# Kernel optimization log

Measured on AMD Instinct MI355X. Metric: run time of the kernel, lower is better.

Reference implementation:

```python
import jax, jax.numpy as jnp
import numpy as np

D_MODEL = 1024
D_STATE = 128
EXPAND = 2
HEADDIM = 64
D_CONV = 4
VAR_NUM = 3
D_INNER = EXPAND * D_MODEL            # 2048
NHEADS = D_INNER // HEADDIM           # 32
CONV_DIM = D_INNER + 2 * D_STATE      # 2304 (x, B, C share the conv)
D_IN_PROJ = 2 * D_INNER + 2 * D_STATE + NHEADS  # 4384


def setup_inputs() -> dict:
    key = jax.random.key(0)
    ks = jax.random.split(key, 10)
    s = 0.02
    B, L = 4, 2048
    return {
        "h_prev": jax.random.normal(ks[0], (B, L, D_MODEL), jnp.float32),
        "emb_next": jax.random.normal(ks[1], (B, L, D_MODEL), jnp.float32),
        "norm_w": jnp.ones((D_MODEL,), jnp.float32),
        "proj_W": jax.random.normal(ks[2], (D_MODEL, 2 * D_MODEL), jnp.float32) * s,
        "proj_b": jnp.zeros((D_MODEL,), jnp.float32),
        "in_proj_W": jax.random.normal(ks[3], (D_IN_PROJ, D_MODEL), jnp.float32) * s,
        "conv_w": jax.random.normal(ks[4], (CONV_DIM, D_CONV), jnp.float32) * s,
        "conv_b": jnp.zeros((CONV_DIM,), jnp.float32),
        "dt_bias": jax.random.uniform(ks[5], (NHEADS,), jnp.float32) * 0.1,
        "A_log": jnp.log(jnp.arange(1, NHEADS + 1, dtype=jnp.float32)),
        "D": jnp.ones((NHEADS,), jnp.float32),
        "gnorm_w": jnp.ones((D_INNER,), jnp.float32),
        "out_proj_W": jax.random.normal(ks[6], (D_MODEL, D_INNER), jnp.float32) * s,
        "dec_W": jax.random.normal(ks[7], (VAR_NUM, D_MODEL), jnp.float32) * s,
        "dec_b": jnp.zeros((VAR_NUM,), jnp.float32),
    }


def rmsnorm(x, w, eps=1e-6):
    xf = x.astype(jnp.float32)
    v = jnp.mean(jnp.square(xf), axis=-1, keepdims=True)
    return w * (xf * jax.lax.rsqrt(v + eps)).astype(x.dtype)


def gated_rmsnorm(y, z, w, eps=1e-5):
    y = y * jax.nn.silu(z)
    v = jnp.mean(jnp.square(y.astype(jnp.float32)), axis=-1, keepdims=True)
    return w * (y.astype(jnp.float32) * jax.lax.rsqrt(v + eps)).astype(y.dtype)


def mamba2(u, in_proj_W, conv_w, conv_b, dt_bias, A_log, D, gnorm_w, out_proj_W):
    B, L, _ = u.shape
    zxbcdt = u @ in_proj_W.T  # [B,L,D_IN_PROJ]
    z, xBC, dt = jnp.split(zxbcdt, [D_INNER, D_INNER + CONV_DIM], axis=-1)
    # causal depthwise conv over time
    lhs = jnp.moveaxis(xBC, -1, 1)               # [B,C,L]
    rhs = conv_w[:, None, :]                     # [C,1,K]
    conv = jax.lax.conv_general_dilated(lhs, rhs, (1,), [(D_CONV - 1, 0)],
                                        feature_group_count=CONV_DIM)
    xBC = jax.nn.silu(jnp.moveaxis(conv, 1, -1) + conv_b)
    x, Bm, Cm = jnp.split(xBC, [D_INNER, D_INNER + D_STATE], axis=-1)
    x = x.reshape(B, L, NHEADS, HEADDIM)         # [B,L,H,P]
    dt = jax.nn.softplus(dt + dt_bias)           # [B,L,H]
    A = -jnp.exp(A_log)                          # [H]
    dA = jnp.exp(dt * A)                         # [B,L,H]

    def step(state, inp):
        dA_t, dt_t, B_t, C_t, x_t = inp          # [B,H],[B,H],[B,N],[B,N],[B,H,P]
        state = state * dA_t[..., None, None] + (dt_t[..., None, None] * x_t[..., None]) * B_t[:, None, None, :]
        y_t = jnp.einsum('bhpn,bn->bhp', state, C_t)
        return state, y_t

    init = jnp.zeros((B, NHEADS, HEADDIM, D_STATE), u.dtype)
    xs = (jnp.moveaxis(dA, 1, 0), jnp.moveaxis(dt, 1, 0), jnp.moveaxis(Bm, 1, 0),
          jnp.moveaxis(Cm, 1, 0), jnp.moveaxis(x, 1, 0))
    _, y = jax.lax.scan(step, init, xs)          # y: [L,B,H,P]
    y = jnp.moveaxis(y, 0, 1) + D[None, None, :, None] * x
    y = y.reshape(B, L, D_INNER)
    y = gated_rmsnorm(y, z, gnorm_w)
    return y @ out_proj_W.T                      # [B,L,D_MODEL]


def reference(h_prev, emb_next, norm_w, proj_W, proj_b, in_proj_W, conv_w, conv_b,
              dt_bias, A_log, D, gnorm_w, out_proj_W, dec_W, dec_b):
    combined = jnp.concatenate([rmsnorm(h_prev, norm_w), rmsnorm(emb_next, norm_w)], axis=-1)
    h_prime = combined @ proj_W.T + proj_b       # [B,L,D_MODEL]
    h_k = mamba2(h_prime, in_proj_W, conv_w, conv_b, dt_bias, A_log, D, gnorm_w, out_proj_W)
    output = h_k @ dec_W.T + dec_b               # [B,L,VAR_NUM]
    return output, h_k
```

## Files before the change

kernel.cpp:

```cpp
#include <hip/hip_runtime.h>
#include <stdint.h>

#define T_TOK 8192
#define SEQL  2048
#define DM    1024
#define DI    2048
#define DSTATE 128
#define NH    32
#define HD    64
#define CONVD 2304
#define DINP  4384
#define LD_ZX 4480
#define QC    64
#define NCH   32

typedef __attribute__((ext_vector_type(8))) __bf16 bfrag;
typedef __attribute__((ext_vector_type(8))) short s16x8;
typedef __attribute__((ext_vector_type(4))) float f32x4;

__device__ __forceinline__ float bf2f(unsigned short u){
  return __uint_as_float(((unsigned)u) << 16);
}
__device__ __forceinline__ unsigned short f2bf(float f){
  unsigned u = __float_as_uint(f);
  unsigned r = (u + 0x7FFFu + ((u >> 16) & 1u)) >> 16;
  return (unsigned short)r;
}

__device__ __forceinline__ void gl_lds16(const unsigned short* g, unsigned short* l){
  __builtin_amdgcn_global_load_lds(
      (const __attribute__((address_space(1))) void*)g,
      (__attribute__((address_space(3))) void*)l,
      16, 0, 0);
}
__device__ __forceinline__ void gl_lds4(const float* g, float* l){
  __builtin_amdgcn_global_load_lds(
      (const __attribute__((address_space(1))) void*)g,
      (__attribute__((address_space(3))) void*)l,
      4, 0, 0);
}

__global__ __launch_bounds__(256) void prep_kernel(const float* __restrict__ s0,
                                                   const float* __restrict__ s1,
                                                   const float* __restrict__ s2,
                                                   unsigned short* __restrict__ d0,
                                                   unsigned short* __restrict__ d1,
                                                   unsigned short* __restrict__ d2,
                                                   const float* __restrict__ a,
                                                   const float* __restrict__ b,
                                                   const float* __restrict__ w,
                                                   unsigned short* __restrict__ out){
  int blk = blockIdx.x;
  int tid = threadIdx.x;
  if (blk < 8576){
    const float* src; unsigned short* dst; int i, srcn4;
    if (blk < 2048){
      src = s0; dst = d0; i = blk * 256 + tid; srcn4 = DM * DI / 4;
    } else if (blk < 6528){
      src = s1; dst = d1; i = (blk - 2048) * 256 + tid; srcn4 = DINP * DM / 4;
    } else {
      src = s2; dst = d2; i = (blk - 6528) * 256 + tid; srcn4 = DM * DI / 4;
    }
    ushort4 o;
    if (i < srcn4){
      float4 v = ((const float4*)src)[i];
      o.x = f2bf(v.x); o.y = f2bf(v.y); o.z = f2bf(v.z); o.w = f2bf(v.w);
    } else {
      o.x = o.y = o.z = o.w = 0;
    }
    *(ushort4*)(dst + (size_t)i * 4) = o;
    return;
  }
  int t = blk - 8576;
  float4 va = *(const float4*)(a + (size_t)t * DM + tid * 4);
  float4 vb = *(const float4*)(b + (size_t)t * DM + tid * 4);
  float sa = va.x*va.x + va.y*va.y + va.z*va.z + va.w*va.w;
  float sb = vb.x*vb.x + vb.y*vb.y + vb.z*vb.z + vb.w*vb.w;
  #pragma unroll
  for (int o = 32; o; o >>= 1){ sa += __shfl_down(sa, o); sb += __shfl_down(sb, o); }
  __shared__ float reda[4], redb[4];
  int wv = tid >> 6, lane = tid & 63;
  if (!lane){ reda[wv] = sa; redb[wv] = sb; }
  __syncthreads();
  float ta = reda[0] + reda[1] + reda[2] + reda[3];
  float tb = redb[0] + redb[1] + redb[2] + redb[3];
  float ra = rsqrtf(ta * (1.f/1024.f) + 1e-6f);
  float rb = rsqrtf(tb * (1.f/1024.f) + 1e-6f);
  float4 vw = *(const float4*)(w + tid * 4);
  unsigned short* o0 = out + (size_t)t * DI + tid * 4;
  o0[0] = f2bf(va.x*ra*vw.x); o0[1] = f2bf(va.y*ra*vw.y);
  o0[2] = f2bf(va.z*ra*vw.z); o0[3] = f2bf(va.w*ra*vw.w);
  unsigned short* o1 = o0 + DM;
  o1[0] = f2bf(vb.x*rb*vw.x); o1[1] = f2bf(vb.y*rb*vw.y);
  o1[2] = f2bf(vb.z*rb*vw.z); o1[3] = f2bf(vb.w*rb*vw.w);
}

template<bool F32OUT>
__global__ __launch_bounds__(256) void gemm_bf16_kernel(const unsigned short* __restrict__ A,
                                                        const unsigned short* __restrict__ W,
                                                        void* __restrict__ Cv,
                                                        const float* __restrict__ bias,
                                                        int M, int N, int K, int ldc){
  __shared__ unsigned short As[128 * 64];
  __shared__ unsigned short Bs[128 * 64];
  const int nN = N >> 7;
  int bid = blockIdx.x;
  const int cpx = gridDim.x >> 3;
  bid = (bid & 7) * cpx + (bid >> 3);
  const int tm = bid / nN, tn = bid % nN;
  const int tid = threadIdx.x;
  const int wv = tid >> 6, lane = tid & 63;
  const int wm = wv >> 1, wn = wv & 1;
  const int rA = lane >> 3;
  const int cS = ((lane & 7) ^ rA) << 3;
  const size_t arow0 = (size_t)(tm * 128) * K;
  const size_t brow0 = (size_t)(tn * 128) * K;

  int aoff[4][2], boff[4][2];
  #pragma unroll
  for (int f = 0; f < 4; ++f)
    #pragma unroll
    for (int kk = 0; kk < 2; ++kk){
      int ar = wm*64 + f*16 + (lane & 15);
      int br = wn*64 + f*16 + (lane & 15);
      int u  = kk*4 + (lane >> 4);
      aoff[f][kk] = ar * 64 + ((u ^ (ar & 7)) << 3);
      boff[f][kk] = br * 64 + ((u ^ (br & 7)) << 3);
    }

  f32x4 zero4 = {0.f, 0.f, 0.f, 0.f};
  f32x4 acc[4][4];
  #pragma unroll
  for (int i = 0; i < 4; ++i)
    #pragma unroll
    for (int j = 0; j < 4; ++j) acc[i][j] = zero4;

  const int nK = K >> 6;
  for (int kt = 0; kt < nK; ++kt){
    const int k0 = kt << 6;
    if (kt) __syncthreads();
    #pragma unroll
    for (int i = 0; i < 4; ++i){
      int base = (wv * 4 + i) * 8;
      gl_lds16(A + arow0 + (size_t)(base + rA) * K + k0 + cS, &As[base * 64]);
      gl_lds16(W + brow0 + (size_t)(base + rA) * K + k0 + cS, &Bs[base * 64]);
    }
    __syncthreads();
    #pragma unroll
    for (int kk = 0; kk < 2; ++kk){
      bfrag af[4], bfv[4];
      #pragma unroll
      for (int f = 0; f < 4; ++f){
        af[f]  = *reinterpret_cast<const bfrag*>(&As[aoff[f][kk]]);
        bfv[f] = *reinterpret_cast<const bfrag*>(&Bs[boff[f][kk]]);
      }
      #pragma unroll
      for (int fm = 0; fm < 4; ++fm)
        #pragma unroll
        for (int fn = 0; fn < 4; ++fn)
          acc[fm][fn] = __builtin_amdgcn_mfma_f32_16x16x32_bf16(af[fm], bfv[fn], acc[fm][fn], 0, 0, 0);
    }
  }
  const int r0 = (lane >> 4) * 4, ci = lane & 15;
  #pragma unroll
  for (int fm = 0; fm < 4; ++fm){
    #pragma unroll
    for (int fn = 0; fn < 4; ++fn){
      int col = tn*128 + wn*64 + fn*16 + ci;
      float bv = bias ? bias[col] : 0.f;
      #pragma unroll
      for (int r = 0; r < 4; ++r){
        int row = tm*128 + wm*64 + fm*16 + r0 + r;
        float val = acc[fm][fn][r] + bv;
        if (F32OUT) ((float*)Cv)[(size_t)row * ldc + col] = val;
        else        ((unsigned short*)Cv)[(size_t)row * ldc + col] = f2bf(val);
      }
    }
  }
}

__global__ __launch_bounds__(256) void convcum_kernel(const unsigned short* __restrict__ zx,
                                                      const float* __restrict__ cw,
                                                      const float* __restrict__ cb,
                                                      unsigned short* __restrict__ xbc,
                                                      const float* __restrict__ dtbias,
                                                      const float* __restrict__ alog,
                                                      float* __restrict__ cumT,
                                                      float* __restrict__ dtT,
                                                      float* __restrict__ decayG){
  int blk = blockIdx.x;
  int tid = threadIdx.x;
  if (blk < 4608){
    int c = (blk % 9) * 256 + tid;
    int tg = (blk / 9) * 16;
    int l0 = tg & (SEQL - 1);
    const unsigned short* base = zx + (size_t)tg * LD_ZX + DI + c;
    float v[19];
    #pragma unroll
    for (int i = 0; i < 19; ++i){
      int ll = l0 - 3 + i;
      v[i] = (ll >= 0) ? bf2f(base[(ptrdiff_t)(i - 3) * LD_ZX]) : 0.f;
    }
    float w0 = cw[c*4+0], w1 = cw[c*4+1], w2 = cw[c*4+2], w3 = cw[c*4+3];
    float cbv = cb[c];
    unsigned short* ob = xbc + (size_t)tg * CONVD + c;
    #pragma unroll
    for (int s = 0; s < 16; ++s){
      float acc = cbv + w0*v[s] + w1*v[s+1] + w2*v[s+2] + w3*v[s+3];
      float sv = acc / (1.f + expf(-acc));
      ob[(size_t)s * CONVD] = f2bf(sv);
    }
    return;
  }
  int gw = (blk - 4608) * 4 + (tid >> 6);
  int l = tid & 63;
  int c = gw & 31, h = (gw >> 5) & 31, b = gw >> 10;
  size_t t = (size_t)b * SEQL + c * QC + l;
  float xr = bf2f(zx[t * LD_ZX + 4352 + h]) + dtbias[h];
  float dt = (xr > 20.f) ? xr : log1pf(expf(xr));
  float A = -expf(alog[h]);
  float x = dt * A;
  #pragma unroll
  for (int d = 1; d < 64; d <<= 1){
    float y = __shfl_up(x, d);
    if (l >= d) x += y;
  }
  size_t o = ((size_t)(b * NH + h)) * SEQL + c * QC + l;
  cumT[o] = x;
  dtT[o] = dt;
  float tot = __shfl(x, 63);
  if (l == 0) decayG[(b * NH + h) * NCH + c] = expf(tot);
}

__global__ __launch_bounds__(256) void chunk_dS_kernel(const unsigned short* __restrict__ xbc,
                                                       const float* __restrict__ cumT,
                                                       const float* __restrict__ dtT,
                                                       unsigned short* __restrict__ dS){
  __shared__ unsigned short Xw[64 * 64];
  __shared__ unsigned short Bt[128 * 64];
  __shared__ float cumS[64], dtS[64];
  const int blk = blockIdx.x;
  const int c = blk & 31, h = (blk >> 5) & 31, b = blk >> 10;
  const int tid = threadIdx.x;
  const int wv = tid >> 6, l = tid & 63;
  const size_t tokB = (size_t)b * SEQL + c * QC;
  const int bh = b * NH + h;

  if (wv == 0) gl_lds4(cumT + (size_t)bh * SEQL + c * QC + l, cumS);
  if (wv == 1) gl_lds4(dtT  + (size_t)bh * SEQL + c * QC + l, dtS);

  const int j = tid >> 2, g4 = tid & 3;
  const unsigned short* xsrc = xbc + (tokB + j) * CONVD + h * HD + g4 * 16;
  s16x8 x0 = *(const s16x8*)xsrc, x1 = *(const s16x8*)(xsrc + 8);
  const unsigned short* bsrc = xbc + (tokB + j) * CONVD + DI + g4 * 32;
  s16x8 b0 = *(const s16x8*)bsrc,        b1 = *(const s16x8*)(bsrc + 8);
  s16x8 b2 = *(const s16x8*)(bsrc + 16), b3 = *(const s16x8*)(bsrc + 24);
  __syncthreads();

  float wj = expf(cumS[63] - cumS[j]) * dtS[j];
  const int jh = (j >> 3), jl = (j & 7);
  #pragma unroll
  for (int e = 0; e < 8; ++e){
    int p = g4 * 16 + e;
    Xw[p * 64 + ((jh ^ (p & 7)) << 3) + jl] = f2bf(bf2f((unsigned short)x0[e]) * wj);
    int p2 = p + 8;
    Xw[p2 * 64 + ((jh ^ (p2 & 7)) << 3) + jl] = f2bf(bf2f((unsigned short)x1[e]) * wj);
  }
  #pragma unroll
  for (int e = 0; e < 8; ++e){
    int n0 = g4 * 32 + e;
    Bt[(n0     ) * 64 + ((jh ^ ((n0     ) & 7)) << 3) + jl] = (unsigned short)b0[e];
    Bt[(n0 +  8) * 64 + ((jh ^ ((n0 +  8) & 7)) << 3) + jl] = (unsigned short)b1[e];
    Bt[(n0 + 16) * 64 + ((jh ^ ((n0 + 16) & 7)) << 3) + jl] = (unsigned short)b2[e];
    Bt[(n0 + 24) * 64 + ((jh ^ ((n0 + 24) & 7)) << 3) + jl] = (unsigned short)b3[e];
  }
  __syncthreads();

  f32x4 z4 = {0.f,0.f,0.f,0.f};
  f32x4 acc[4][2];
  #pragma unroll
  for (int pt = 0; pt < 4; ++pt){ acc[pt][0] = z4; acc[pt][1] = z4; }
  #pragma unroll
  for (int ks = 0; ks < 2; ++ks){
    const int au = ((ks * 4 + (l >> 4)) ^ (l & 7));
    bfrag a[4], bb[2];
    #pragma unroll
    for (int pt = 0; pt < 4; ++pt)
      a[pt] = *(const bfrag*)&Xw[(pt * 16 + (l & 15)) * 64 + au * 8];
    #pragma unroll
    for (int nt = 0; nt < 2; ++nt)
      bb[nt] = *(const bfrag*)&Bt[((wv * 2 + nt) * 16 + (l & 15)) * 64 + au * 8];
    #pragma unroll
    for (int pt = 0; pt < 4; ++pt)
      #pragma unroll
      for (int nt = 0; nt < 2; ++nt)
        acc[pt][nt] = __builtin_amdgcn_mfma_f32_16x16x32_bf16(a[pt], bb[nt], acc[pt][nt], 0, 0, 0);
  }
  unsigned short* out = dS + ((size_t)(bh * NCH + c) * 64) * 128;
  #pragma unroll
  for (int pt = 0; pt < 4; ++pt)
    #pragma unroll
    for (int nt = 0; nt < 2; ++nt)
      #pragma unroll
      for (int r = 0; r < 4; ++r){
        int p = pt * 16 + (l >> 4) * 4 + r;
        int n = (wv * 2 + nt) * 16 + (l & 15);
        out[(size_t)p * 128 + n] = f2bf(acc[pt][nt][r]);
      }
}

__global__ __launch_bounds__(256) void chunk_state_kernel(const float* __restrict__ decayG,
                                                          unsigned short* __restrict__ dS){
  int i = blockIdx.x * 256 + threadIdx.x;
  int n8 = i & 15, p = (i >> 4) & 63, bh = i >> 10;
  float s[8];
  #pragma unroll
  for (int j = 0; j < 8; ++j) s[j] = 0.f;
  const float* dg = decayG + bh * NCH;
  for (int c = 0; c < NCH; ++c){
    size_t idx = ((size_t)(bh * NCH + c) * 64 + p) * 128 + n8 * 8;
    s16x8 d = *(const s16x8*)(dS + idx);
    s16x8 o;
    #pragma unroll
    for (int j = 0; j < 8; ++j) o[j] = (short)f2bf(s[j]);
    *(s16x8*)(dS + idx) = o;
    float g = dg[c];
    #pragma unroll
    for (int j = 0; j < 8; ++j) s[j] = fmaf(g, s[j], bf2f((unsigned short)d[j]));
  }
}

__global__ __launch_bounds__(256) void chunk_Y_kernel(const unsigned short* __restrict__ xbc,
                                                      const unsigned short* __restrict__ Sb,
                                                      const float* __restrict__ cumT,
                                                      const float* __restrict__ dtT,
                                                      const float* __restrict__ Dvec,
                                                      unsigned short* __restrict__ ybuf){
  __shared__ unsigned short Cs[64 * 128];
  __shared__ unsigned short Bs[64 * 128];
  __shared__ unsigned short Xt[64 * 64];
  __shared__ unsigned short Ms[64 * 64];
  __shared__ float cumS[64], dtS[64];
  const int blk = blockIdx.x;
  const int c = blk & 31, h = (blk >> 5) & 31, b = blk >> 10;
  const int tid = threadIdx.x;
  const int wv = tid >> 6, l = tid & 63;
  const size_t tokB = (size_t)b * SEQL + c * QC;
  const int bh = b * NH + h;

  #pragma unroll
  for (int kk = 0; kk < 4; ++kk){
    int k = wv * 4 + kk;
    int row = k * 4 + (l >> 4);
    int us = (l & 15) ^ (row & 7);
    gl_lds16(xbc + (tokB + row) * CONVD + 2176 + us * 8, &Cs[k * 512]);
    gl_lds16(xbc + (tokB + row) * CONVD + 2048 + us * 8, &Bs[k * 512]);
  }
  if (wv == 0) gl_lds4(cumT + (size_t)bh * SEQL + c * QC + l, cumS);
  if (wv == 1) gl_lds4(dtT  + (size_t)bh * SEQL + c * QC + l, dtS);

  {
    const int j = tid >> 2, g4 = tid & 3;
    const unsigned short* xsrc = xbc + (tokB + j) * CONVD + h * HD + g4 * 16;
    s16x8 x0 = *(const s16x8*)xsrc, x1 = *(const s16x8*)(xsrc + 8);
    const int jh = j >> 3, jl = j & 7;
    #pragma unroll
    for (int e = 0; e < 8; ++e){
      int p = g4 * 16 + e;
      Xt[p * 64 + ((jh ^ (p & 7)) << 3) + jl] = (unsigned short)x0[e];
      int p2 = p + 8;
      Xt[p2 * 64 + ((jh ^ (p2 & 7)) << 3) + jl] = (unsigned short)x1[e];
    }
  }
  __syncthreads();

  bfrag sbf[4][4];
  {
    const unsigned short* sbase = Sb + (size_t)(bh * NCH + c) * 64 * 128;
    #pragma unroll
    for (int pt = 0; pt < 4; ++pt)
      #pragma unroll
      for (int ks = 0; ks < 4; ++ks){
        int p = pt * 16 + (l & 15);
        sbf[pt][ks] = *(const bfrag*)(sbase + (size_t)p * 128 + ks * 32 + (l >> 4) * 8);
      }
  }

  f32x4 z4 = {0.f,0.f,0.f,0.f};
  f32x4 macc[4] = {z4, z4, z4, z4};
  #pragma unroll
  for (int ks = 0; ks < 4; ++ks){
    const int au = (ks * 4 + (l >> 4)) ^ (l & 7);
    bfrag ca = *(const bfrag*)&Cs[(wv * 16 + (l & 15)) * 128 + au * 8];
    #pragma unroll
    for (int jt = 0; jt < 4; ++jt){
      bfrag bb = *(const bfrag*)&Bs[(jt * 16 + (l & 15)) * 128 + au * 8];
      macc[jt] = __builtin_amdgcn_mfma_f32_16x16x32_bf16(ca, bb, macc[jt], 0, 0, 0);
    }
  }
  float cj[4], dj[4];
  #pragma unroll
  for (int jt = 0; jt < 4; ++jt){
    int jv = jt * 16 + (l & 15);
    cj[jt] = cumS[jv]; dj[jt] = dtS[jv];
  }
  float ctv[4];
  #pragma unroll
  for (int r = 0; r < 4; ++r) ctv[r] = cumS[wv * 16 + (l >> 4) * 4 + r];
  #pragma unroll
  for (int jt = 0; jt < 4; ++jt){
    int jv = jt * 16 + (l & 15);
    #pragma unroll
    for (int r = 0; r < 4; ++r){
      int tb = wv * 16 + (l >> 4) * 4 + r;
      float g = (jv <= tb) ? expf(ctv[r] - cj[jt]) * dj[jt] : 0.f;
      Ms[tb * 64 + (((jv >> 3) ^ (tb & 7)) << 3) + (jv & 7)] = f2bf(macc[jt][r] * g);
    }
  }
  f32x4 yacc[4] = {z4, z4, z4, z4};
  #pragma unroll
  for (int kj = 0; kj < 2; ++kj){
    const int au = (kj * 4 + (l >> 4)) ^ (l & 7);
    bfrag ma = *(const bfrag*)&Ms[(wv * 16 + (l & 15)) * 64 + au * 8];
    #pragma unroll
    for (int pt = 0; pt < 4; ++pt){
      bfrag wx = *(const bfrag*)&Xt[(pt * 16 + (l & 15)) * 64 + au * 8];
      yacc[pt] = __builtin_amdgcn_mfma_f32_16x16x32_bf16(ma, wx, yacc[pt], 0, 0, 0);
    }
  }
  f32x4 iacc[4] = {z4, z4, z4, z4};
  #pragma unroll
  for (int ks = 0; ks < 4; ++ks){
    const int au = (ks * 4 + (l >> 4)) ^ (l & 7);
    bfrag ca = *(const bfrag*)&Cs[(wv * 16 + (l & 15)) * 128 + au * 8];
    #pragma unroll
    for (int pt = 0; pt < 4; ++pt)
      iacc[pt] = __builtin_amdgcn_mfma_f32_16x16x32_bf16(ca, sbf[pt][ks], iacc[pt], 0, 0, 0);
  }
  const float Dh = Dvec[h];
  float er[4];
  #pragma unroll
  for (int r = 0; r < 4; ++r) er[r] = expf(ctv[r]);
  #pragma unroll
  for (int pt = 0; pt < 4; ++pt)
    #pragma unroll
    for (int r = 0; r < 4; ++r){
      int p = pt * 16 + (l & 15);
      int tb = wv * 16 + (l >> 4) * 4 + r;
      float xv = bf2f(Xt[p * 64 + (((tb >> 3) ^ (p & 7)) << 3) + (tb & 7)]);
      float yv = yacc[pt][r] + er[r] * iacc[pt][r] + Dh * xv;
      ybuf[(tokB + tb) * DI + h * HD + p] = f2bf(yv);
    }
}

__global__ __launch_bounds__(256) void gated_kernel(const unsigned short* __restrict__ y,
                                                    const unsigned short* __restrict__ zx,
                                                    const float* __restrict__ gw,
                                                    unsigned short* __restrict__ out){
  int t = blockIdx.x, tid = threadIdx.x;
  s16x8 yv = *(const s16x8*)(y  + (size_t)t * DI    + tid * 8);
  s16x8 zv = *(const s16x8*)(zx + (size_t)t * LD_ZX + tid * 8);
  float g[8]; float ss = 0.f;
  #pragma unroll
  for (int j = 0; j < 8; ++j){
    float yf = bf2f((unsigned short)yv[j]);
    float zf = bf2f((unsigned short)zv[j]);
    float gi = yf * (zf / (1.f + expf(-zf)));
    g[j] = gi; ss += gi * gi;
  }
  #pragma unroll
  for (int o = 32; o; o >>= 1) ss += __shfl_down(ss, o);
  __shared__ float red[4];
  int wv = tid >> 6, lane = tid & 63;
  if (!lane) red[wv] = ss;
  __syncthreads();
  float tot = red[0] + red[1] + red[2] + red[3];
  float sc = rsqrtf(tot * (1.f/2048.f) + 1e-5f);
  unsigned short* o0 = out + (size_t)t * DI + tid * 8;
  #pragma unroll
  for (int j = 0; j < 8; ++j) o0[j] = f2bf(g[j] * sc * gw[tid * 8 + j]);
}

__global__ __launch_bounds__(256) void dec_kernel(const float* __restrict__ hk,
                                                  const float* __restrict__ dw,
                                                  const float* __restrict__ db,
                                                  float* __restrict__ out){
  int t = (blockIdx.x * 256 + threadIdx.x) >> 6;
  int lane = threadIdx.x & 63;
  const float* hr = hk + (size_t)t * DM + lane * 16;
  float h[16];
  #pragma unroll
  for (int j = 0; j < 16; ++j) h[j] = hr[j];
  float a0 = 0.f, a1 = 0.f, a2 = 0.f;
  const float* w0 = dw + lane * 16;
  const float* w1 = dw + DM + lane * 16;
  const float* w2 = dw + 2 * DM + lane * 16;
  #pragma unroll
  for (int j = 0; j < 16; ++j){
    a0 = fmaf(h[j], w0[j], a0);
    a1 = fmaf(h[j], w1[j], a1);
    a2 = fmaf(h[j], w2[j], a2);
  }
  #pragma unroll
  for (int o = 32; o; o >>= 1){
    a0 += __shfl_down(a0, o);
    a1 += __shfl_down(a1, o);
    a2 += __shfl_down(a2, o);
  }
  if (!lane){
    out[t * 3 + 0] = a0 + db[0];
    out[t * 3 + 1] = a1 + db[1];
    out[t * 3 + 2] = a2 + db[2];
  }
}

extern "C" void kernel_launch(void* const* d_in, const int* in_sizes, int n_in,
                              void* d_out, int out_size, void* d_ws, size_t ws_size,
                              hipStream_t stream){
  const float* h_prev    = (const float*)d_in[0];
  const float* emb_next  = (const float*)d_in[1];
  const float* norm_w    = (const float*)d_in[2];
  const float* proj_W    = (const float*)d_in[3];
  const float* proj_b    = (const float*)d_in[4];
  const float* in_proj_W = (const float*)d_in[5];
  const float* conv_w    = (const float*)d_in[6];
  const float* conv_b    = (const float*)d_in[7];
  const float* dt_bias   = (const float*)d_in[8];
  const float* A_log     = (const float*)d_in[9];
  const float* Dvec      = (const float*)d_in[10];
  const float* gnorm_w   = (const float*)d_in[11];
  const float* out_proj_W= (const float*)d_in[12];
  const float* dec_W     = (const float*)d_in[13];
  const float* dec_b     = (const float*)d_in[14];

  char* ws = (char*)d_ws;
  size_t off = 0;
  auto take = [&](size_t bytes){ char* p = ws + off; off += (bytes + 255) & ~(size_t)255; return p; };
  unsigned short* wproj = (unsigned short*)take((size_t)DM * DI * 2);
  unsigned short* winp  = (unsigned short*)take((size_t)LD_ZX * DM * 2);
  unsigned short* wout  = (unsigned short*)take((size_t)DM * DI * 2);
  unsigned short* zx    = (unsigned short*)take((size_t)T_TOK * LD_ZX * 2);
  float*          cumT  = (float*)take((size_t)4 * NH * SEQL * 4);
  float*          dtT   = (float*)take((size_t)4 * NH * SEQL * 4);
  float*          decayG= (float*)take((size_t)4 * NH * NCH * 4);
  char* regionA = take((size_t)T_TOK * CONVD * 2);
  unsigned short* combined = (unsigned short*)regionA;
  unsigned short* xbc      = (unsigned short*)regionA;
  char* regionY = take((size_t)T_TOK * DI * 2);
  unsigned short* hprime = (unsigned short*)regionY;
  unsigned short* ybuf   = (unsigned short*)regionY;
  unsigned short* dS = (unsigned short*)take((size_t)128 * NCH * 64 * 128 * 2);

  float* outp = (float*)d_out;
  float* hk   = outp + (size_t)T_TOK * 3;

  prep_kernel<<<16768, 256, 0, stream>>>(proj_W, in_proj_W, out_proj_W,
                                         wproj, winp, wout,
                                         h_prev, emb_next, norm_w, combined);

  gemm_bf16_kernel<false><<<(T_TOK/128)*(DM/128), 256, 0, stream>>>(combined, wproj, hprime, proj_b,
                                                                    T_TOK, DM, DI, DM);
  gemm_bf16_kernel<false><<<(T_TOK/128)*(LD_ZX/128), 256, 0, stream>>>(hprime, winp, zx, nullptr,
                                                                       T_TOK, LD_ZX, DM, LD_ZX);
  convcum_kernel<<<5632, 256, 0, stream>>>(zx, conv_w, conv_b, xbc,
                                           dt_bias, A_log, cumT, dtT, decayG);
  chunk_dS_kernel<<<4096, 256, 0, stream>>>(xbc, cumT, dtT, dS);
  chunk_state_kernel<<<512, 256, 0, stream>>>(decayG, dS);
  chunk_Y_kernel<<<4096, 256, 0, stream>>>(xbc, dS, cumT, dtT, Dvec, ybuf);
  gated_kernel<<<T_TOK, 256, 0, stream>>>(ybuf, zx, gnorm_w, ybuf);
  gemm_bf16_kernel<true><<<(T_TOK/128)*(DM/128), 256, 0, stream>>>(ybuf, wout, hk, nullptr,
                                                                   T_TOK, DM, DI, DM);
  dec_kernel<<<T_TOK/4, 256, 0, stream>>>(hk, dec_W, dec_b, outp);
}
```

Baseline: 349.3 us.

## Fuse decoder projection into out_proj GEMM epilogue and remap tiles per XCD

The separate dec_kernel is removed. The 3-way decoder dot product is now computed in the out_proj GEMM epilogue by reducing each row's partial sums across lanes and adding them into the output with atomics. The bias initialisation moves into gated_kernel. The GEMM block-to-tile mapping also changes so each XCD owns a band of 8 row tiles, walked in column groups of GN, to improve L2 reuse. This saves one launch and one re-read of h_k, at the cost of atomic contention (8 column tiles per row) and non-deterministic summation order.

```diff
diff --git a/kernel.cpp b/kernel.cpp
--- a/kernel.cpp
+++ b/kernel.cpp
@@ -95,19 +95,22 @@
   o1[2] = f2bf(vb.z*rb*vw.z); o1[3] = f2bf(vb.w*rb*vw.w);
 }
 
-template<bool F32OUT>
+template<bool F32OUT, bool DECF>
 __global__ __launch_bounds__(256) void gemm_bf16_kernel(const unsigned short* __restrict__ A,
                                                         const unsigned short* __restrict__ W,
                                                         void* __restrict__ Cv,
                                                         const float* __restrict__ bias,
-                                                        int M, int N, int K, int ldc){
+                                                        const float* __restrict__ dw,
+                                                        float* __restrict__ outd,
+                                                        int M, int N, int K, int ldc, int GN){
   __shared__ unsigned short As[128 * 64];
   __shared__ unsigned short Bs[128 * 64];
   const int nN = N >> 7;
-  int bid = blockIdx.x;
-  const int cpx = gridDim.x >> 3;
-  bid = (bid & 7) * cpx + (bid >> 3);
-  const int tm = bid / nN, tn = bid % nN;
+  const int xcd = blockIdx.x & 7, cc = blockIdx.x >> 3;
+  const int gsz = 8 * GN;
+  const int grp = cc / gsz, rem = cc % gsz;
+  const int tm = xcd * 8 + rem / GN;
+  const int tn = grp * GN + rem % GN;
   const int tid = threadIdx.x;
   const int wv = tid >> 6, lane = tid & 63;
   const int wm = wv >> 1, wn = wv & 1;
@@ -162,18 +165,44 @@
     }
   }
   const int r0 = (lane >> 4) * 4, ci = lane & 15;
+  float dwr[3][4];
+  if (DECF){
+    #pragma unroll
+    for (int v = 0; v < 3; ++v)
+      #pragma unroll
+      for (int fn = 0; fn < 4; ++fn)
+        dwr[v][fn] = dw[v * DM + tn*128 + wn*64 + fn*16 + ci];
+  }
   #pragma unroll
   for (int fm = 0; fm < 4; ++fm){
     #pragma unroll
-    for (int fn = 0; fn < 4; ++fn){
-      int col = tn*128 + wn*64 + fn*16 + ci;
-      float bv = bias ? bias[col] : 0.f;
-      #pragma unroll
-      for (int r = 0; r < 4; ++r){
-        int row = tm*128 + wm*64 + fm*16 + r0 + r;
-        float val = acc[fm][fn][r] + bv;
+    for (int r = 0; r < 4; ++r){
+      const int row = tm*128 + wm*64 + fm*16 + r0 + r;
+      float pd0 = 0.f, pd1 = 0.f, pd2 = 0.f;
+      #pragma unroll
+      for (int fn = 0; fn < 4; ++fn){
+        const int col = tn*128 + wn*64 + fn*16 + ci;
+        float val = acc[fm][fn][r] + (bias ? bias[col] : 0.f);
         if (F32OUT) ((float*)Cv)[(size_t)row * ldc + col] = val;
         else        ((unsigned short*)Cv)[(size_t)row * ldc + col] = f2bf(val);
+        if (DECF){
+          pd0 = fmaf(val, dwr[0][fn], pd0);
+          pd1 = fmaf(val, dwr[1][fn], pd1);
+          pd2 = fmaf(val, dwr[2][fn], pd2);
+        }
+      }
+      if (DECF){
+        #pragma unroll
+        for (int m = 1; m < 16; m <<= 1){
+          pd0 += __shfl_xor(pd0, m);
+          pd1 += __shfl_xor(pd1, m);
+          pd2 += __shfl_xor(pd2, m);
+        }
+        if (ci == 0){
+          atomicAdd(&outd[row * 3 + 0], pd0);
+          atomicAdd(&outd[row * 3 + 1], pd1);
+          atomicAdd(&outd[row * 3 + 2], pd2);
+        }
       }
     }
   }
@@ -456,8 +485,11 @@
 __global__ __launch_bounds__(256) void gated_kernel(const unsigned short* __restrict__ y,
                                                     const unsigned short* __restrict__ zx,
                                                     const float* __restrict__ gw,
-                                                    unsigned short* __restrict__ out){
+                                                    unsigned short* __restrict__ out,
+                                                    const float* __restrict__ db,
+                                                    float* __restrict__ outd){
   int t = blockIdx.x, tid = threadIdx.x;
+  if (tid < 3) outd[t * 3 + tid] = db[tid];
   s16x8 yv = *(const s16x8*)(y  + (size_t)t * DI    + tid * 8);
   s16x8 zv = *(const s16x8*)(zx + (size_t)t * LD_ZX + tid * 8);
   float g[8]; float ss = 0.f;
@@ -479,39 +511,6 @@
   unsigned short* o0 = out + (size_t)t * DI + tid * 8;
   #pragma unroll
   for (int j = 0; j < 8; ++j) o0[j] = f2bf(g[j] * sc * gw[tid * 8 + j]);
-}
-
-__global__ __launch_bounds__(256) void dec_kernel(const float* __restrict__ hk,
-                                                  const float* __restrict__ dw,
-                                                  const float* __restrict__ db,
-                                                  float* __restrict__ out){
-  int t = (blockIdx.x * 256 + threadIdx.x) >> 6;
-  int lane = threadIdx.x & 63;
-  const float* hr = hk + (size_t)t * DM + lane * 16;
-  float h[16];
-  #pragma unroll
-  for (int j = 0; j < 16; ++j) h[j] = hr[j];
-  float a0 = 0.f, a1 = 0.f, a2 = 0.f;
-  const float* w0 = dw + lane * 16;
-  const float* w1 = dw + DM + lane * 16;
-  const float* w2 = dw + 2 * DM + lane * 16;
-  #pragma unroll
-  for (int j = 0; j < 16; ++j){
-    a0 = fmaf(h[j], w0[j], a0);
-    a1 = fmaf(h[j], w1[j], a1);
-    a2 = fmaf(h[j], w2[j], a2);
-  }
-  #pragma unroll
-  for (int o = 32; o; o >>= 1){
-    a0 += __shfl_down(a0, o);
-    a1 += __shfl_down(a1, o);
-    a2 += __shfl_down(a2, o);
-  }
-  if (!lane){
-    out[t * 3 + 0] = a0 + db[0];
-    out[t * 3 + 1] = a1 + db[1];
-    out[t * 3 + 2] = a2 + db[2];
-  }
 }
 
 extern "C" void kernel_launch(void* const* d_in, const int* in_sizes, int n_in,
@@ -558,17 +557,16 @@
                                          wproj, winp, wout,
                                          h_prev, emb_next, norm_w, combined);
 
-  gemm_bf16_kernel<false><<<(T_TOK/128)*(DM/128), 256, 0, stream>>>(combined, wproj, hprime, proj_b,
-                                                                    T_TOK, DM, DI, DM);
-  gemm_bf16_kernel<false><<<(T_TOK/128)*(LD_ZX/128), 256, 0, stream>>>(hprime, winp, zx, nullptr,
-                                                                       T_TOK, LD_ZX, DM, LD_ZX);
+  gemm_bf16_kernel<false,false><<<(T_TOK/128)*(DM/128), 256, 0, stream>>>(
+      combined, wproj, hprime, proj_b, nullptr, nullptr, T_TOK, DM, DI, DM, 8);
+  gemm_bf16_kernel<false,false><<<(T_TOK/128)*(LD_ZX/128), 256, 0, stream>>>(
+      hprime, winp, zx, nullptr, nullptr, nullptr, T_TOK, LD_ZX, DM, LD_ZX, 5);
   convcum_kernel<<<5632, 256, 0, stream>>>(zx, conv_w, conv_b, xbc,
                                            dt_bias, A_log, cumT, dtT, decayG);
   chunk_dS_kernel<<<4096, 256, 0, stream>>>(xbc, cumT, dtT, dS);
   chunk_state_kernel<<<512, 256, 0, stream>>>(decayG, dS);
   chunk_Y_kernel<<<4096, 256, 0, stream>>>(xbc, dS, cumT, dtT, Dvec, ybuf);
-  gated_kernel<<<T_TOK, 256, 0, stream>>>(ybuf, zx, gnorm_w, ybuf);
-  gemm_bf16_kernel<true><<<(T_TOK/128)*(DM/128), 256, 0, stream>>>(ybuf, wout, hk, nullptr,
-                                                                   T_TOK, DM, DI, DM);
-  dec_kernel<<<T_TOK/4, 256, 0, stream>>>(hk, dec_W, dec_b, outp);
-}
+  gated_kernel<<<T_TOK, 256, 0, stream>>>(ybuf, zx, gnorm_w, ybuf, dec_b, outp);
+  gemm_bf16_kernel<true,true><<<(T_TOK/128)*(DM/128), 256, 0, stream>>>(
+      ybuf, wout, hk, nullptr, dec_W, outp, T_TOK, DM, DI, DM, 8);
+}
```

Measured after the change: 371.3 us. 6.3% more time.
